# Kernel optimization log

Measured on AMD Instinct MI355X. Metric: run time of the kernel, lower is better.

The kernel has to match this reference:

```python
import jax, jax.numpy as jnp
import numpy as np

HEADS = 16
EMBED = 1024
HEAD_DIM = EMBED // HEADS


def setup_inputs() -> dict:
    key = jax.random.key(0)
    ks = jax.random.split(key, 11)
    B, S, E = 4, 2048, EMBED
    s = 1.0 / np.sqrt(E)
    return {
        "query": jax.random.normal(ks[0], (B, S, E), jnp.float32),
        "key": jax.random.normal(ks[1], (B, S, E), jnp.float32),
        "value": jax.random.normal(ks[2], (B, S, E), jnp.float32),
        "Wq": jax.random.normal(ks[3], (E, E), jnp.float32) * s,
        "bq": jax.random.normal(ks[4], (E,), jnp.float32) * s,
        "Wk": jax.random.normal(ks[5], (E, E), jnp.float32) * s,
        "bk": jax.random.normal(ks[6], (E,), jnp.float32) * s,
        "Wv": jax.random.normal(ks[7], (E, E), jnp.float32) * s,
        "bv": jax.random.normal(ks[8], (E,), jnp.float32) * s,
        "Wo": jax.random.normal(ks[9], (E, E), jnp.float32) * s,
        "bo": jax.random.normal(ks[10], (E,), jnp.float32) * s,
    }


def reference(query, key, value, Wq, bq, Wk, bk, Wv, bv, Wo, bo):
    B, Sq, E = query.shape
    Sk = key.shape[1]
    H, D = HEADS, HEAD_DIM
    # linear projections (torch Linear: x @ W.T + b)
    q = (query @ Wq.T + bq).reshape(B, Sq, H, D)
    k = (key @ Wk.T + bk).reshape(B, Sk, H, D)
    v = (value @ Wv.T + bv).reshape(B, Sk, H, D)
    scores = jnp.einsum("bqhd,bkhd->bhqk", q, k) / np.sqrt(D).astype(jnp.float32)
    attn = jax.nn.softmax(scores, axis=-1)
    out = jnp.einsum("bhqk,bkhd->bqhd", attn, v).reshape(B, Sq, E)
    # dropout p=0.0 -> identity
    return out @ Wo.T + bo
```

## Files before the change

kernel.cpp:

```cpp
#include <hip/hip_runtime.h>
#include <hip/hip_bf16.h>
#include <stdint.h>

#define BATCH 4
#define SEQ   2048
#define EMB   1024
#define NHEAD 16
#define HDIM  64

typedef __bf16 bf16x8 __attribute__((ext_vector_type(8)));
typedef float  f32x4  __attribute__((ext_vector_type(4)));
typedef float  f32x16 __attribute__((ext_vector_type(16)));

__global__ __launch_bounds__(256) void cvt_f32_bf16(const float* __restrict__ in,
                                                    __bf16* __restrict__ out, int n4) {
  int i = blockIdx.x * 256 + threadIdx.x;
  if (i >= n4) return;
  float4 v = reinterpret_cast<const float4*>(in)[i];
  union { ushort4 u; __bf16 b[4]; } o;
  o.b[0] = (__bf16)v.x; o.b[1] = (__bf16)v.y;
  o.b[2] = (__bf16)v.z; o.b[3] = (__bf16)v.w;
  reinterpret_cast<ushort4*>(out)[i] = o.u;
}

__device__ __forceinline__ void gload_lds16(const void* g, void* l) {
  __builtin_amdgcn_global_load_lds((const uint32_t __attribute__((address_space(1)))*)g,
                                   (uint32_t __attribute__((address_space(3)))*)l, 16, 0, 0);
}

enum { EPI_BF16 = 0, EPI_F32 = 1, EPI_VT = 2 };

template <int MODE>
__global__ __launch_bounds__(256, 2)
void gemm_bt(const __bf16* __restrict__ A, const __bf16* __restrict__ Bt,
             const float* __restrict__ bias, void* __restrict__ Cout,
             int M, int N, int K) {
  __shared__ __bf16 As[128 * 32];
  __shared__ __bf16 Bs[128 * 32];
  const int tid  = threadIdx.x;
  const int wave = tid >> 6, lane = tid & 63;
  const int l4 = lane >> 4, l15 = lane & 15;
  const int row0 = blockIdx.x * 128, col0 = blockIdx.y * 128;
  const int wr = (wave >> 1) * 64, wc = (wave & 1) * 64;

  const int srow = wave * 16 + (lane >> 2);
  const int scol = (lane & 3) * 8;

  f32x4 acc[4][4] = {};

  const __bf16* ga = A  + (size_t)(row0 + srow) * K + scol;
  const __bf16* gb = Bt + (size_t)(col0 + srow) * K + scol;
  char* lA = (char*)As + wave * 1024;
  char* lB = (char*)Bs + wave * 1024;

  for (int k0 = 0; k0 < K; k0 += 32) {
    __syncthreads();
    gload_lds16(ga + k0, lA);
    gload_lds16(ga + k0 + (size_t)64 * K, lA + 4096);
    gload_lds16(gb + k0, lB);
    gload_lds16(gb + k0 + (size_t)64 * K, lB + 4096);
    __syncthreads();

    bf16x8 af[4], bfv[4];
#pragma unroll
    for (int m = 0; m < 4; ++m)
      af[m] = *(const bf16x8*)((const char*)As + (wr + m * 16 + l15) * 64 + l4 * 16);
#pragma unroll
    for (int n = 0; n < 4; ++n)
      bfv[n] = *(const bf16x8*)((const char*)Bs + (wc + n * 16 + l15) * 64 + l4 * 16);
#pragma unroll
    for (int m = 0; m < 4; ++m)
#pragma unroll
      for (int n = 0; n < 4; ++n)
        acc[m][n] = __builtin_amdgcn_mfma_f32_16x16x32_bf16(af[m], bfv[n], acc[m][n], 0, 0, 0);
  }

#pragma unroll
  for (int m = 0; m < 4; ++m) {
    const int r = row0 + wr + m * 16 + l4 * 4;
#pragma unroll
    for (int n = 0; n < 4; ++n) {
      const int c  = col0 + wc + n * 16 + l15;
      const float bb = bias[c];
      if (MODE == EPI_F32) {
        float* C = (float*)Cout;
#pragma unroll
        for (int i = 0; i < 4; ++i) C[(size_t)(r + i) * N + c] = acc[m][n][i] + bb;
      } else if (MODE == EPI_BF16) {
        __bf16* C = (__bf16*)Cout;
#pragma unroll
        for (int i = 0; i < 4; ++i) C[(size_t)(r + i) * N + c] = (__bf16)(acc[m][n][i] + bb);
      } else {
        const int b = r >> 11, s = r & (SEQ - 1);
        const int h = c >> 6, d = c & (HDIM - 1);
        union { ushort4 u; __bf16 x[4]; } o;
#pragma unroll
        for (int i = 0; i < 4; ++i) o.x[i] = (__bf16)(acc[m][n][i] + bb);
        *(ushort4*)((__bf16*)Cout + ((size_t)((b * NHEAD + h) * HDIM + d)) * SEQ + s) = o.u;
      }
    }
  }
}

__device__ __forceinline__ f32x16 mfma32(bf16x8 a, bf16x8 b, f32x16 c) {
  return __builtin_amdgcn_mfma_f32_32x32x16_bf16(a, b, c, 0, 0, 0);
}

__global__ __launch_bounds__(512, 2)
void attn_fwd2(const __bf16* __restrict__ Q, const __bf16* __restrict__ Kk,
               const __bf16* __restrict__ Vt, __bf16* __restrict__ O) {
  __shared__ __bf16 Ks[2][64 * 64];
  __shared__ __bf16 Vs[2][64 * 64];

  const int tid = threadIdx.x;
  const int w = tid >> 6, lane = tid & 63;
  const int l31 = lane & 31, hi = lane >> 5;
  const int bh = blockIdx.x, b = bh >> 4, h = bh & 15;
  const int q0 = blockIdx.y * 256 + w * 32;

  bf16x8 qf[4];
  {
    const __bf16* qb = Q + (size_t)(b * SEQ + q0 + l31) * EMB + h * HDIM + hi * 8;
#pragma unroll
    for (int ks = 0; ks < 4; ++ks) {
      bf16x8 t = *(const bf16x8*)(qb + ks * 16);
#pragma unroll
      for (int j = 0; j < 8; ++j) t[j] = (__bf16)((float)t[j] * 0.125f);
      qf[ks] = t;
    }
  }

  const int srow = w * 8 + (lane >> 3);
  const int sswz = ((lane & 7) * 16) ^ ((srow & 7) << 4);
  const char* kg = (const char*)(Kk + (size_t)(b * SEQ) * EMB + h * HDIM)
                   + (size_t)srow * (EMB * 2) + sswz;
  const char* vg = (const char*)(Vt + (size_t)((b * NHEAD + h) * HDIM) * SEQ)
                   + (size_t)srow * (SEQ * 2) + sswz;

  auto STAGE = [&](int bi, int t) {
    gload_lds16(kg + (size_t)t * (64 * EMB * 2), (char*)&Ks[bi][0] + w * 1024);
    gload_lds16(vg + (size_t)t * 128,            (char*)&Vs[bi][0] + w * 1024);
  };

  f32x16 oacc0 = {}, oacc1 = {};
  float mx = -1e30f, ls = 0.f;
  const int rswz = (l31 & 7) << 4;

  STAGE(0, 0);
  for (int t = 0; t < 32; ++t) {
    const int bi = t & 1;
    if (t < 31) {
      STAGE(bi ^ 1, t + 1);
      asm volatile("s_waitcnt vmcnt(2)" ::: "memory");
    } else {
      asm volatile("s_waitcnt vmcnt(0)" ::: "memory");
    }
    __builtin_amdgcn_s_barrier();
    __builtin_amdgcn_sched_barrier(0);

    f32x16 sc0 = {}, sc1 = {};
    const char* kb = (const char*)&Ks[bi][0];
#pragma unroll
    for (int ks = 0; ks < 4; ++ks) {
      const int o = (ks * 32 + hi * 16) ^ rswz;
      bf16x8 k0 = *(const bf16x8*)(kb + l31 * 128 + o);
      bf16x8 k1 = *(const bf16x8*)(kb + (l31 + 32) * 128 + o);
      sc0 = mfma32(k0, qf[ks], sc0);
      sc1 = mfma32(k1, qf[ks], sc1);
    }

    float pm = sc0[0];
#pragma unroll
    for (int r = 1; r < 16; ++r) pm = fmaxf(pm, sc0[r]);
#pragma unroll
    for (int r = 0; r < 16; ++r) pm = fmaxf(pm, sc1[r]);
    pm = fmaxf(pm, __shfl_xor(pm, 32));
    const float mn = fmaxf(mx, pm);
    const float corr = __expf(mx - mn);
    mx = mn;
    float rs = 0.f;
#pragma unroll
    for (int r = 0; r < 16; ++r) { sc0[r] = __expf(sc0[r] - mn); rs += sc0[r]; }
#pragma unroll
    for (int r = 0; r < 16; ++r) { sc1[r] = __expf(sc1[r] - mn); rs += sc1[r]; }
    rs += __shfl_xor(rs, 32);
    ls = ls * corr + rs;
#pragma unroll
    for (int r = 0; r < 16; ++r) { oacc0[r] *= corr; oacc1[r] *= corr; }

    union Fu { uint32_t w[4]; bf16x8 v; };
    auto pk = [](float a, float b) -> uint32_t {
      union { __bf16 h[2]; uint32_t u; } z;
      z.h[0] = (__bf16)a; z.h[1] = (__bf16)b; return z.u;
    };
    bf16x8 pa[4];
    {
      uint32_t A0 = pk(sc0[0], sc0[1]),  A1 = pk(sc0[2], sc0[3]);
      uint32_t B0 = pk(sc0[4], sc0[5]),  B1 = pk(sc0[6], sc0[7]);
      uint32_t C0 = pk(sc0[8], sc0[9]),  C1 = pk(sc0[10], sc0[11]);
      uint32_t D0 = pk(sc0[12], sc0[13]), D1 = pk(sc0[14], sc0[15]);
      uint32_t sA0 = __shfl_xor((int)A0, 32), sA1 = __shfl_xor((int)A1, 32);
      uint32_t sB0 = __shfl_xor((int)B0, 32), sB1 = __shfl_xor((int)B1, 32);
      uint32_t sC0 = __shfl_xor((int)C0, 32), sC1 = __shfl_xor((int)C1, 32);
      uint32_t sD0 = __shfl_xor((int)D0, 32), sD1 = __shfl_xor((int)D1, 32);
      Fu f0, f1;
      f0.w[0] = hi ? sB0 : A0;  f0.w[1] = hi ? sB1 : A1;
      f0.w[2] = hi ? B0 : sA0;  f0.w[3] = hi ? B1 : sA1;
      f1.w[0] = hi ? sD0 : C0;  f1.w[1] = hi ? sD1 : C1;
      f1.w[2] = hi ? D0 : sC0;  f1.w[3] = hi ? D1 : sC1;
      pa[0] = f0.v; pa[1] = f1.v;
      uint32_t E0 = pk(sc1[0], sc1[1]),  E1 = pk(sc1[2], sc1[3]);
      uint32_t F0 = pk(sc1[4], sc1[5]),  F1 = pk(sc1[6], sc1[7]);
      uint32_t G0 = pk(sc1[8], sc1[9]),  G1 = pk(sc1[10], sc1[11]);
      uint32_t H0 = pk(sc1[12], sc1[13]), H1 = pk(sc1[14], sc1[15]);
      uint32_t sE0 = __shfl_xor((int)E0, 32), sE1 = __shfl_xor((int)E1, 32);
      uint32_t sF0 = __shfl_xor((int)F0, 32), sF1 = __shfl_xor((int)F1, 32);
      uint32_t sG0 = __shfl_xor((int)G0, 32), sG1 = __shfl_xor((int)G1, 32);
      uint32_t sH0 = __shfl_xor((int)H0, 32), sH1 = __shfl_xor((int)H1, 32);
      Fu f2, f3;
      f2.w[0] = hi ? sF0 : E0;  f2.w[1] = hi ? sF1 : E1;
      f2.w[2] = hi ? F0 : sE0;  f2.w[3] = hi ? F1 : sE1;
      f3.w[0] = hi ? sH0 : G0;  f3.w[1] = hi ? sH1 : G1;
      f3.w[2] = hi ? H0 : sG0;  f3.w[3] = hi ? H1 : sG1;
      pa[2] = f2.v; pa[3] = f3.v;
    }

    const char* vb = (const char*)&Vs[bi][0];
#pragma unroll
    for (int ks = 0; ks < 4; ++ks) {
      const int o = (ks * 32 + hi * 16) ^ rswz;
      bf16x8 v0 = *(const bf16x8*)(vb + l31 * 128 + o);
      bf16x8 v1 = *(const bf16x8*)(vb + (l31 + 32) * 128 + o);
      oacc0 = mfma32(v0, pa[ks], oacc0);
      oacc1 = mfma32(v1, pa[ks], oacc1);
    }

    __builtin_amdgcn_s_barrier();
    __builtin_amdgcn_sched_barrier(0);
  }

  const float inv = 1.f / ls;
  __bf16* ob = O + (size_t)(b * SEQ + q0 + l31) * EMB + h * HDIM;
#pragma unroll
  for (int c = 0; c < 4; ++c) {
    union { ushort4 u; __bf16 x[4]; } o0, o1;
#pragma unroll
    for (int i = 0; i < 4; ++i) {
      o0.x[i] = (__bf16)(oacc0[4 * c + i] * inv);
      o1.x[i] = (__bf16)(oacc1[4 * c + i] * inv);
    }
    *(ushort4*)(ob + 8 * c + 4 * hi)      = o0.u;
    *(ushort4*)(ob + 32 + 8 * c + 4 * hi) = o1.u;
  }
}

extern "C" void kernel_launch(void* const* d_in, const int* in_sizes, int n_in,
                              void* d_out, int out_size, void* d_ws, size_t ws_size,
                              hipStream_t stream) {
  const float* query = (const float*)d_in[0];
  const float* key   = (const float*)d_in[1];
  const float* value = (const float*)d_in[2];
  const float* Wq = (const float*)d_in[3]; const float* bq = (const float*)d_in[4];
  const float* Wk = (const float*)d_in[5]; const float* bk = (const float*)d_in[6];
  const float* Wv = (const float*)d_in[7]; const float* bv = (const float*)d_in[8];
  const float* Wo = (const float*)d_in[9]; const float* bo = (const float*)d_in[10];

  char* ws = (char*)d_ws;
  const size_t MB = 1u << 20;
  __bf16* Xb  = (__bf16*)(ws);
  __bf16* Qb  = (__bf16*)(ws + 16 * MB);
  __bf16* Kb  = (__bf16*)(ws + 32 * MB);
  __bf16* Vt  = (__bf16*)(ws + 48 * MB);
  __bf16* Wqb = (__bf16*)(ws + 64 * MB);
  __bf16* Wkb = (__bf16*)(ws + 66 * MB);
  __bf16* Wvb = (__bf16*)(ws + 68 * MB);
  __bf16* Wob = (__bf16*)(ws + 70 * MB);

  const int NE = BATCH * SEQ * EMB;
  const int NW = EMB * EMB;
  const int M = BATCH * SEQ;

  dim3 blk(256);
  dim3 gg(M / 128, EMB / 128);

  cvt_f32_bf16<<<dim3(NW / 4 / 256), blk, 0, stream>>>(Wq, Wqb, NW / 4);
  cvt_f32_bf16<<<dim3(NW / 4 / 256), blk, 0, stream>>>(Wk, Wkb, NW / 4);
  cvt_f32_bf16<<<dim3(NW / 4 / 256), blk, 0, stream>>>(Wv, Wvb, NW / 4);
  cvt_f32_bf16<<<dim3(NW / 4 / 256), blk, 0, stream>>>(Wo, Wob, NW / 4);

  cvt_f32_bf16<<<dim3(NE / 4 / 256), blk, 0, stream>>>(query, Xb, NE / 4);
  gemm_bt<EPI_BF16><<<gg, blk, 0, stream>>>(Xb, Wqb, bq, Qb, M, EMB, EMB);
  cvt_f32_bf16<<<dim3(NE / 4 / 256), blk, 0, stream>>>(key, Xb, NE / 4);
  gemm_bt<EPI_BF16><<<gg, blk, 0, stream>>>(Xb, Wkb, bk, Kb, M, EMB, EMB);
  cvt_f32_bf16<<<dim3(NE / 4 / 256), blk, 0, stream>>>(value, Xb, NE / 4);
  gemm_bt<EPI_VT><<<gg, blk, 0, stream>>>(Xb, Wvb, bv, Vt, M, EMB, EMB);

  attn_fwd2<<<dim3(BATCH * NHEAD, SEQ / 256), dim3(512), 0, stream>>>(Qb, Kb, Vt, Xb);

  gemm_bt<EPI_F32><<<gg, blk, 0, stream>>>(Xb, Wob, bo, d_out, M, EMB, EMB);
}
```

Measured before the change: 383.2 us.

## Rewrite projection GEMM with double-buffered swizzled LDS and exp2-based softmax

The projection GEMM becomes a 512-thread kernel with a 256x128 tile and a K-step of 64. LDS is double-buffered and XOR-swizzled, so the next tile's global-to-LDS load overlaps the current tile's MFMAs, and wave priority is raised around the MFMA block. The attention kernel folds log2(e) into the Q scale and uses exp2f instead of __expf. The larger LDS footprint and register use may limit occupancy.

```diff
diff --git a/kernel.cpp b/kernel.cpp
--- a/kernel.cpp
+++ b/kernel.cpp
@@ -31,48 +31,80 @@
 enum { EPI_BF16 = 0, EPI_F32 = 1, EPI_VT = 2 };
 
 template <int MODE>
-__global__ __launch_bounds__(256, 2)
-void gemm_bt(const __bf16* __restrict__ A, const __bf16* __restrict__ Bt,
-             const float* __restrict__ bias, void* __restrict__ Cout,
-             int M, int N, int K) {
-  __shared__ __bf16 As[128 * 32];
-  __shared__ __bf16 Bs[128 * 32];
+__global__ __launch_bounds__(512, 2)
+void gemm2(const __bf16* __restrict__ A, const __bf16* __restrict__ Bt,
+           const float* __restrict__ bias, void* __restrict__ Cout,
+           int M, int N, int K) {
+  __shared__ __bf16 As[2][256 * 64];
+  __shared__ __bf16 Bs[2][128 * 64];
+
   const int tid  = threadIdx.x;
   const int wave = tid >> 6, lane = tid & 63;
   const int l4 = lane >> 4, l15 = lane & 15;
-  const int row0 = blockIdx.x * 128, col0 = blockIdx.y * 128;
+  const int row0 = blockIdx.x * 256, col0 = blockIdx.y * 128;
   const int wr = (wave >> 1) * 64, wc = (wave & 1) * 64;
 
-  const int srow = wave * 16 + (lane >> 2);
-  const int scol = (lane & 3) * 8;
+  const int sr = tid >> 3;
+  const int scb = ((tid & 7) * 16) ^ ((sr & 7) << 4);
+  const char* gA = (const char*)A  + ((size_t)(row0 + sr) * K) * 2 + scb;
+  const char* gB = (const char*)Bt + ((size_t)(col0 + sr) * K) * 2 + scb;
+  const size_t rstride = (size_t)64 * K * 2;
 
   f32x4 acc[4][4] = {};
 
-  const __bf16* ga = A  + (size_t)(row0 + srow) * K + scol;
-  const __bf16* gb = Bt + (size_t)(col0 + srow) * K + scol;
-  char* lA = (char*)As + wave * 1024;
-  char* lB = (char*)Bs + wave * 1024;
-
-  for (int k0 = 0; k0 < K; k0 += 32) {
-    __syncthreads();
-    gload_lds16(ga + k0, lA);
-    gload_lds16(ga + k0 + (size_t)64 * K, lA + 4096);
-    gload_lds16(gb + k0, lB);
-    gload_lds16(gb + k0 + (size_t)64 * K, lB + 4096);
-    __syncthreads();
-
-    bf16x8 af[4], bfv[4];
+  auto STAGE = [&](int bi, int t) {
+    char* lA = (char*)&As[bi][0] + wave * 1024;
+    char* lB = (char*)&Bs[bi][0] + wave * 1024;
+    const size_t ko = (size_t)t * 128;
+#pragma unroll
+    for (int c = 0; c < 4; ++c)
+      gload_lds16(gA + ko + c * rstride, lA + c * 8192);
+#pragma unroll
+    for (int c = 0; c < 2; ++c)
+      gload_lds16(gB + ko + c * rstride, lB + c * 8192);
+  };
+
+  const int NT = K >> 6;
+  STAGE(0, 0);
+  asm volatile("s_waitcnt vmcnt(0)" ::: "memory");
+  __builtin_amdgcn_s_barrier();
+  __builtin_amdgcn_sched_barrier(0);
+
+  const int swz = (l15 & 7) << 4;
+  int cur = 0;
+  for (int t = 0; t < NT; ++t) {
+    if (t + 1 < NT) STAGE(cur ^ 1, t + 1);
+
+    const char* la = (const char*)&As[cur][0];
+    const char* lb = (const char*)&Bs[cur][0];
+    bf16x8 af[4][2], bfv[4][2];
 #pragma unroll
     for (int m = 0; m < 4; ++m)
-      af[m] = *(const bf16x8*)((const char*)As + (wr + m * 16 + l15) * 64 + l4 * 16);
+#pragma unroll
+      for (int k = 0; k < 2; ++k)
+        af[m][k] = *(const bf16x8*)(la + (wr + m * 16 + l15) * 128 + ((k * 64 + l4 * 16) ^ swz));
 #pragma unroll
     for (int n = 0; n < 4; ++n)
-      bfv[n] = *(const bf16x8*)((const char*)Bs + (wc + n * 16 + l15) * 64 + l4 * 16);
-#pragma unroll
-    for (int m = 0; m < 4; ++m)
-#pragma unroll
-      for (int n = 0; n < 4; ++n)
-        acc[m][n] = __builtin_amdgcn_mfma_f32_16x16x32_bf16(af[m], bfv[n], acc[m][n], 0, 0, 0);
+#pragma unroll
+      for (int k = 0; k < 2; ++k)
+        bfv[n][k] = *(const bf16x8*)(lb + (wc + n * 16 + l15) * 128 + ((k * 64 + l4 * 16) ^ swz));
+
+    asm volatile("s_waitcnt lgkmcnt(0)" ::: "memory");
+    __builtin_amdgcn_sched_barrier(0);
+    __builtin_amdgcn_s_setprio(1);
+#pragma unroll
+    for (int k = 0; k < 2; ++k)
+#pragma unroll
+      for (int m = 0; m < 4; ++m)
+#pragma unroll
+        for (int n = 0; n < 4; ++n)
+          acc[m][n] = __builtin_amdgcn_mfma_f32_16x16x32_bf16(af[m][k], bfv[n][k], acc[m][n], 0, 0, 0);
+    __builtin_amdgcn_s_setprio(0);
+
+    asm volatile("s_waitcnt vmcnt(0)" ::: "memory");
+    __builtin_amdgcn_s_barrier();
+    __builtin_amdgcn_sched_barrier(0);
+    cur ^= 1;
   }
 
 #pragma unroll
@@ -125,7 +157,7 @@
     for (int ks = 0; ks < 4; ++ks) {
       bf16x8 t = *(const bf16x8*)(qb + ks * 16);
 #pragma unroll
-      for (int j = 0; j < 8; ++j) t[j] = (__bf16)((float)t[j] * 0.125f);
+      for (int j = 0; j < 8; ++j) t[j] = (__bf16)((float)t[j] * 0.1803368801111244f);
       qf[ks] = t;
     }
   }
@@ -176,13 +208,13 @@
     for (int r = 0; r < 16; ++r) pm = fmaxf(pm, sc1[r]);
     pm = fmaxf(pm, __shfl_xor(pm, 32));
     const float mn = fmaxf(mx, pm);
-    const float corr = __expf(mx - mn);
+    const float corr = exp2f(mx - mn);
     mx = mn;
     float rs = 0.f;
 #pragma unroll
-    for (int r = 0; r < 16; ++r) { sc0[r] = __expf(sc0[r] - mn); rs += sc0[r]; }
-#pragma unroll
-    for (int r = 0; r < 16; ++r) { sc1[r] = __expf(sc1[r] - mn); rs += sc1[r]; }
+    for (int r = 0; r < 16; ++r) { sc0[r] = exp2f(sc0[r] - mn); rs += sc0[r]; }
+#pragma unroll
+    for (int r = 0; r < 16; ++r) { sc1[r] = exp2f(sc1[r] - mn); rs += sc1[r]; }
     rs += __shfl_xor(rs, 32);
     ls = ls * corr + rs;
 #pragma unroll
@@ -281,7 +313,8 @@
   const int M = BATCH * SEQ;
 
   dim3 blk(256);
-  dim3 gg(M / 128, EMB / 128);
+  dim3 gg(M / 256, EMB / 128);
+  dim3 gblk(512);
 
   cvt_f32_bf16<<<dim3(NW / 4 / 256), blk, 0, stream>>>(Wq, Wqb, NW / 4);
   cvt_f32_bf16<<<dim3(NW / 4 / 256), blk, 0, stream>>>(Wk, Wkb, NW / 4);
@@ -289,13 +322,13 @@
   cvt_f32_bf16<<<dim3(NW / 4 / 256), blk, 0, stream>>>(Wo, Wob, NW / 4);
 
   cvt_f32_bf16<<<dim3(NE / 4 / 256), blk, 0, stream>>>(query, Xb, NE / 4);
-  gemm_bt<EPI_BF16><<<gg, blk, 0, stream>>>(Xb, Wqb, bq, Qb, M, EMB, EMB);
+  gemm2<EPI_BF16><<<gg, gblk, 0, stream>>>(Xb, Wqb, bq, Qb, M, EMB, EMB);
   cvt_f32_bf16<<<dim3(NE / 4 / 256), blk, 0, stream>>>(key, Xb, NE / 4);
-  gemm_bt<EPI_BF16><<<gg, blk, 0, stream>>>(Xb, Wkb, bk, Kb, M, EMB, EMB);
+  gemm2<EPI_BF16><<<gg, gblk, 0, stream>>>(Xb, Wkb, bk, Kb, M, EMB, EMB);
   cvt_f32_bf16<<<dim3(NE / 4 / 256), blk, 0, stream>>>(value, Xb, NE / 4);
-  gemm_bt<EPI_VT><<<gg, blk, 0, stream>>>(Xb, Wvb, bv, Vt, M, EMB, EMB);
-
-  attn_fwd2<<<dim3(BATCH * NHEAD, SEQ / 256), dim3(512), 0, stream>>>(Qb, Kb, Vt, Xb);
-
-  gemm_bt<EPI_F32><<<gg, blk, 0, stream>>>(Xb, Wob, bo, d_out, M, EMB, EMB);
-}
+  gemm2<EPI_VT><<<gg, gblk, 0, stream>>>(Xb, Wvb, bv, Vt, M, EMB, EMB);
+
+  attn_fwd2<<<dim3(BATCH * NHEAD, SEQ / 256), gblk, 0, stream>>>(Qb, Kb, Vt, Xb);
+
+  gemm2<EPI_F32><<<gg, gblk, 0, stream>>>(Xb, Wob, bo, d_out, M, EMB, EMB);
+}
```

Result: slower. 413.7 us (+7.9%).
